# Kernel tuning notes

Hardware: AMD Instinct MI355X
Metric: run time of the kernel (lower is better)

The kernel has to match this reference:

```python
import jax, jax.numpy as jnp
import numpy as np

B, S, D = 2, 4096, 512
H, DQK, DV, W = 8, 64, 64, 32
ORDER = 6  # 2^(2*6)=4096 cells: 64x64 Hilbert grid covers max_seq_len=4096


def hilbert_d2xy(d, order):
    """Vectorized standard Hilbert curve d->(x,y) mapping on a 2^order grid."""
    x = jnp.zeros_like(d)
    y = jnp.zeros_like(d)
    t = d
    s = 1
    for _ in range(order):
        rx = (t // 2) & 1
        ry = (t ^ rx) & 1
        swap = ry == 0
        flip = swap & (rx == 1)
        xf = jnp.where(flip, s - 1 - x, x)
        yf = jnp.where(flip, s - 1 - y, y)
        x, y = jnp.where(swap, yf, xf), jnp.where(swap, xf, yf)
        x = x + s * rx
        y = y + s * ry
        t = t // 4
        s = s * 2
    return jnp.stack([x, y], axis=-1)


def neighbor_idx(seq_len, window):
    d = jnp.arange(seq_len, dtype=jnp.int32)
    coords = hilbert_d2xy(d, ORDER).astype(jnp.float32)  # (S, 2)
    diff = coords[:, None, :] - coords[None, :, :]
    dist = jnp.sqrt((diff ** 2).sum(-1))  # (S, S)
    _, idx = jax.lax.top_k(-dist, window)  # k smallest distances
    return idx.astype(jnp.int32)


def setup_inputs() -> dict:
    key = jax.random.key(0)
    k1, k2, k3, k4, k5 = jax.random.split(key, 5)
    sc = float(1.0 / np.sqrt(D))
    return {
        "x": jax.random.normal(k1, (B, S, D), jnp.float32),
        "W_q": jax.random.normal(k2, (H * DQK, D), jnp.float32) * sc,
        "W_k": jax.random.normal(k3, (H * DQK, D), jnp.float32) * sc,
        "W_v": jax.random.normal(k4, (H * DV, D), jnp.float32) * sc,
        "W_o": jax.random.normal(k5, (D, H * DV), jnp.float32) * sc,
        "neighbor_indices": neighbor_idx(S, W),
    }


def reference(x, W_q, W_k, W_v, W_o, neighbor_indices):
    b, s, _ = x.shape
    q = (x @ W_q.T).reshape(b, s, H, DQK).transpose(0, 2, 1, 3)  # (b,h,s,d)
    k = (x @ W_k.T).reshape(b, s, H, DQK).transpose(0, 2, 1, 3)
    v = (x @ W_v.T).reshape(b, s, H, DV).transpose(0, 2, 1, 3)
    kn = k[:, :, neighbor_indices, :]  # gather -> (b,h,s,w,d)
    vn = v[:, :, neighbor_indices, :]
    scale = float(1.0 / np.sqrt(DQK))
    scores = jnp.einsum('bhsd,bhswd->bhsw', q, kn) * scale
    attn = jax.nn.softmax(scores, axis=-1)
    out = jnp.einsum('bhsw,bhswd->bhsd', attn, vn)
    out = out.transpose(0, 2, 1, 3).reshape(b, s, H * DV)
    return out @ W_o.T
```

## Files before the change

kernel.cpp:

```cpp
#include <hip/hip_runtime.h>
#include <hip/hip_bf16.h>
#include <stdint.h>
#include <stddef.h>

constexpr int Bc = 2;
constexpr int Sc = 4096;
constexpr int Dc = 512;
constexpr int Hc = 8;
constexpr int Wc = 32;

using bf16_t = __bf16;
typedef __attribute__((ext_vector_type(8))) __bf16 bf16x8;
typedef __attribute__((ext_vector_type(4))) __bf16 bf16x4;
typedef __attribute__((ext_vector_type(2))) __bf16 bf16x2;
typedef __attribute__((ext_vector_type(4))) float f32x4;

__device__ __forceinline__ void async_copy16(const void* g, void* l) {
    __builtin_amdgcn_global_load_lds(
        (const __attribute__((address_space(1))) void*)g,
        (__attribute__((address_space(3))) void*)l,
        16, 0, 0);
}

__global__ void convert_all(const float* __restrict__ x,
                            const float* __restrict__ wq, const float* __restrict__ wk,
                            const float* __restrict__ wv, const float* __restrict__ wo,
                            bf16_t* __restrict__ xc, bf16_t* __restrict__ dq,
                            bf16_t* __restrict__ dk, bf16_t* __restrict__ dv,
                            bf16_t* __restrict__ dwo) {
    const int blk = blockIdx.x;
    const float* s; bf16_t* d; int base;
    if (blk < 4096) { s = x; d = xc; base = blk * 1024; }
    else {
        const int r = blk - 4096, which = r >> 8;
        s = (which == 0) ? wq : (which == 1) ? wk : (which == 2) ? wv : wo;
        d = (which == 0) ? dq : (which == 1) ? dk : (which == 2) ? dv : dwo;
        base = (r & 255) * 1024;
    }
    const int i = base + threadIdx.x * 4;
    const float4 v = *(const float4*)(s + i);
    bf16x4 o; o[0] = (bf16_t)v.x; o[1] = (bf16_t)v.y;
    o[2] = (bf16_t)v.z; o[3] = (bf16_t)v.w;
    *(bf16x4*)(d + i) = o;
}

template<int BM, int BN, int TM, int TN, bool F32OUT>
__global__ __launch_bounds__(256) void gemm_bt(
    const bf16_t* __restrict__ A, int lda,
    const bf16_t* __restrict__ B0, const bf16_t* __restrict__ B1,
    const bf16_t* __restrict__ B2, int ldb, int nPerB,
    void* __restrict__ C, int ldc, int K)
{
    constexpr int BK = 32;
    __shared__ __align__(1024) bf16_t Alds[BM * BK];
    __shared__ __align__(1024) bf16_t Blds[BN * BK];

    const int tid  = threadIdx.x;
    const int lane = tid & 63;
    const int wv   = tid >> 6;
    const int wm   = wv >> 1;
    const int wn   = wv & 1;
    const int r    = lane & 15;
    const int q4   = lane >> 4;

    const int blkM = blockIdx.x * BM;
    const int colC = blockIdx.y * BN;

    const bf16_t* Bp = B0;
    int nB = colC;
    if (nPerB > 0) {
        int wsel = colC / nPerB;
        nB = colC - wsel * nPerB;
        Bp = (wsel == 0) ? B0 : (wsel == 1) ? B1 : B2;
    }

    f32x4 acc[TM][TN];
    const f32x4 fzero = {0.f, 0.f, 0.f, 0.f};
    #pragma unroll
    for (int i = 0; i < TM; ++i)
        #pragma unroll
        for (int j = 0; j < TN; ++j) acc[i][j] = fzero;

    constexpr int A_LOADS = (BM * BK * 2) / (256 * 16);
    constexpr int B_LOADS = (BN * BK * 2) / (256 * 16);

    for (int kk = 0; kk < K; kk += BK) {
        __syncthreads();
        #pragma unroll
        for (int i = 0; i < A_LOADS; ++i) {
            int off  = i * 4096 + tid * 16;
            int row  = off >> 6;
            int colb = off & 63;
            const char* g = (const char*)A + ((size_t)(blkM + row) * lda + kk) * 2 + colb;
            async_copy16(g, (char*)Alds + off);
        }
        #pragma unroll
        for (int i = 0; i < B_LOADS; ++i) {
            int off  = i * 4096 + tid * 16;
            int row  = off >> 6;
            int colb = off & 63;
            const char* g = (const char*)Bp + ((size_t)(nB + row) * ldb + kk) * 2 + colb;
            async_copy16(g, (char*)Blds + off);
        }
        __syncthreads();

        bf16x8 af[TM], bfr[TN];
        #pragma unroll
        for (int mt = 0; mt < TM; ++mt)
            af[mt] = *(const bf16x8*)&Alds[(wm * TM * 16 + mt * 16 + r) * BK + q4 * 8];
        #pragma unroll
        for (int nt = 0; nt < TN; ++nt)
            bfr[nt] = *(const bf16x8*)&Blds[(wn * TN * 16 + nt * 16 + r) * BK + q4 * 8];

        #pragma unroll
        for (int mt = 0; mt < TM; ++mt)
            #pragma unroll
            for (int nt = 0; nt < TN; ++nt)
                acc[mt][nt] = __builtin_amdgcn_mfma_f32_16x16x32_bf16(
                    af[mt], bfr[nt], acc[mt][nt], 0, 0, 0);
    }

    #pragma unroll
    for (int mt = 0; mt < TM; ++mt) {
        #pragma unroll
        for (int nt = 0; nt < TN; ++nt) {
            int rr0 = blkM + wm * TM * 16 + mt * 16 + q4 * 4;
            int cc  = colC + wn * TN * 16 + nt * 16 + r;
            #pragma unroll
            for (int i = 0; i < 4; ++i) {
                size_t o = (size_t)(rr0 + i) * ldc + cc;
                if constexpr (F32OUT) ((float*)C)[o]  = acc[mt][nt][i];
                else                  ((bf16_t*)C)[o] = (bf16_t)acc[mt][nt][i];
            }
        }
    }
}

__global__ __launch_bounds__(256) void attn_fast(
    const bf16_t* __restrict__ QKV,
    const int*    __restrict__ nidx,
    bf16_t*       __restrict__ attn_out)
{
    __shared__ __align__(16) float wa_lds[4][64];
    const int lane = threadIdx.x & 63;
    const int wv   = threadIdx.x >> 6;

    const int bi  = blockIdx.x;
    const int blk = (bi & 7) * 2048 + (bi >> 3);
    const int wg  = blk * 4 + wv;
    const int s = wg & (Sc - 1);
    const int h = (wg >> 12) & (Hc - 1);
    const int b = wg >> 15;
    const size_t row = (size_t)b * Sc + s;

    const int w    = lane >> 1;
    const int half = lane & 1;
    const int t    = nidx[s * Wc + w];

    const char* qkvB = (const char*)QKV;
    const char* Qptr = qkvB + row * 3072 + h * 128 + half * 64;
    const char* Kptr = qkvB + ((size_t)b * Sc + t) * 3072 + 1024 + h * 128 + half * 64;

    bf16x8 q8[4], k8[4];
    #pragma unroll
    for (int i = 0; i < 4; ++i) {
        q8[i] = *(const bf16x8*)(Qptr + 16 * i);
        k8[i] = *(const bf16x8*)(Kptr + 16 * i);
    }
    float p = 0.f;
    #pragma unroll
    for (int i = 0; i < 4; ++i)
        #pragma unroll
        for (int j = 0; j < 8; ++j)
            p += (float)q8[i][j] * (float)k8[i][j];
    p += __shfl_xor(p, 1);
    p *= 0.125f;

    float mx = p;
    #pragma unroll
    for (int m = 2; m <= 32; m <<= 1) mx = fmaxf(mx, __shfl_xor(mx, m));
    const float e = __expf(p - mx);
    float sum = e;
    #pragma unroll
    for (int m = 2; m <= 32; m <<= 1) sum += __shfl_xor(sum, m);
    const float a = e / sum;

    if (half == 0) {
        wa_lds[wv][2 * w]     = __int_as_float(t * 3072);
        wa_lds[wv][2 * w + 1] = a;
    }
    __syncthreads();

    const int d2 = lane & 31;
    const int nh = lane >> 5;
    const float* chunkp = &wa_lds[wv][nh * 32];
    const char* Vb = qkvB + (size_t)b * Sc * 3072 + 2048 + h * 128;
    const int dk = d2 * 4;

    float acc0 = 0.f, acc1 = 0.f;
    #pragma unroll
    for (int j = 0; j < 8; ++j) {
        const float4 c = *(const float4*)(chunkp + 4 * j);
        {
            const unsigned v = *(const unsigned*)(Vb + __float_as_int(c.x) + dk);
            acc0 = fmaf(c.y, __uint_as_float(v << 16), acc0);
            acc1 = fmaf(c.y, __uint_as_float(v & 0xffff0000u), acc1);
        }
        {
            const unsigned v = *(const unsigned*)(Vb + __float_as_int(c.z) + dk);
            acc0 = fmaf(c.w, __uint_as_float(v << 16), acc0);
            acc1 = fmaf(c.w, __uint_as_float(v & 0xffff0000u), acc1);
        }
    }
    acc0 += __shfl_xor(acc0, 32);
    acc1 += __shfl_xor(acc1, 32);
    if (nh == 0) {
        bf16x2 pr; pr[0] = (bf16_t)acc0; pr[1] = (bf16_t)acc1;
        *(bf16x2*)((char*)attn_out + row * 1024 + h * 128 + dk) = pr;
    }
}

extern "C" void kernel_launch(void* const* d_in, const int* in_sizes, int n_in,
                              void* d_out, int out_size, void* d_ws, size_t ws_size,
                              hipStream_t stream) {
    (void)in_sizes; (void)n_in; (void)out_size; (void)ws_size;
    const int* nidx = (const int*)d_in[5];
    const int M = Bc * Sc;
    float* out = (float*)d_out;

    char* w = (char*)d_ws;
    bf16_t* xc   = (bf16_t*)(w + 256);
    bf16_t* Wqc  = xc  + 4194304;
    bf16_t* Wkc  = Wqc + 262144;
    bf16_t* Wvc  = Wkc + 262144;
    bf16_t* Woc  = Wvc + 262144;
    bf16_t* qkv  = Woc + 262144;
    bf16_t* attnS = xc;

    convert_all<<<5120, 256, 0, stream>>>(
        (const float*)d_in[0], (const float*)d_in[1], (const float*)d_in[2],
        (const float*)d_in[3], (const float*)d_in[4],
        xc, Wqc, Wkc, Wvc, Woc);

    gemm_bt<128, 128, 4, 4, false><<<dim3(M / 128, 1536 / 128), 256, 0, stream>>>(
        xc, Dc, Wqc, Wkc, Wvc, Dc, 512, qkv, 1536, Dc);

    attn_fast<<<(Bc * Hc * Sc) / 4, 256, 0, stream>>>(qkv, nidx, attnS);

    gemm_bt<128, 64, 4, 2, true><<<dim3(M / 128, 512 / 64), 256, 0, stream>>>(
        attnS, 512, Woc, Woc, Woc, 512, 0, out, Dc, Dc);
}
```

Baseline: 146.9 us.

## Restructure neighbor attention lane mapping, drop LDS and barrier, widen out-proj tile

The attention kernel now maps 8 lanes per neighbor over 16-byte dimension chunks, and each lane handles 4 neighbors. K and V are loaded as 16-byte vectors in the same pass. Softmax and the weighted V sum stay in registers using xor shuffles, so the LDS staging buffer and __syncthreads are removed. The output projection GEMM tile grows from 128x64 to 128x128, which halves its grid to 256 blocks and may reduce occupancy across CUs. The new path needs more shuffles to reduce the 8 accumulators.

```diff
diff --git a/kernel.cpp b/kernel.cpp
--- a/kernel.cpp
+++ b/kernel.cpp
@@ -141,7 +141,6 @@
     const int*    __restrict__ nidx,
     bf16_t*       __restrict__ attn_out)
 {
-    __shared__ __align__(16) float wa_lds[4][64];
     const int lane = threadIdx.x & 63;
     const int wv   = threadIdx.x >> 6;
 
@@ -153,70 +152,63 @@
     const int b = wg >> 15;
     const size_t row = (size_t)b * Sc + s;
 
-    const int w    = lane >> 1;
-    const int half = lane & 1;
-    const int t    = nidx[s * Wc + w];
-
-    const char* qkvB = (const char*)QKV;
-    const char* Qptr = qkvB + row * 3072 + h * 128 + half * 64;
-    const char* Kptr = qkvB + ((size_t)b * Sc + t) * 3072 + 1024 + h * 128 + half * 64;
-
-    bf16x8 q8[4], k8[4];
-    #pragma unroll
-    for (int i = 0; i < 4; ++i) {
-        q8[i] = *(const bf16x8*)(Qptr + 16 * i);
-        k8[i] = *(const bf16x8*)(Kptr + 16 * i);
-    }
-    float p = 0.f;
-    #pragma unroll
-    for (int i = 0; i < 4; ++i)
+    const int d8 = lane & 7;
+    const int wq = lane >> 3;
+
+    const char* qkvB  = (const char*)QKV;
+    const bf16x8 q8   = *(const bf16x8*)(qkvB + row * 3072 + h * 128 + d8 * 16);
+    const char* Kbase = qkvB + (size_t)b * Sc * 3072 + 1024 + h * 128 + d8 * 16;
+    const char* Vbase = qkvB + (size_t)b * Sc * 3072 + 2048 + h * 128 + d8 * 16;
+
+    float  p[4];
+    bf16x8 v8s[4];
+    #pragma unroll
+    for (int g = 0; g < 4; ++g) {
+        const int t = nidx[s * Wc + g * 8 + wq];
+        const size_t toff = (size_t)t * 3072;
+        const bf16x8 k8 = *(const bf16x8*)(Kbase + toff);
+        v8s[g] = *(const bf16x8*)(Vbase + toff);
+        float d = 0.f;
+        #pragma unroll
+        for (int j = 0; j < 8; ++j) d += (float)q8[j] * (float)k8[j];
+        d += __shfl_xor(d, 1);
+        d += __shfl_xor(d, 2);
+        d += __shfl_xor(d, 4);
+        p[g] = d * 0.125f;
+    }
+
+    float mx = fmaxf(fmaxf(p[0], p[1]), fmaxf(p[2], p[3]));
+    mx = fmaxf(mx, __shfl_xor(mx, 8));
+    mx = fmaxf(mx, __shfl_xor(mx, 16));
+    mx = fmaxf(mx, __shfl_xor(mx, 32));
+    float e[4];
+    float sum = 0.f;
+    #pragma unroll
+    for (int g = 0; g < 4; ++g) { e[g] = __expf(p[g] - mx); sum += e[g]; }
+    sum += __shfl_xor(sum, 8);
+    sum += __shfl_xor(sum, 16);
+    sum += __shfl_xor(sum, 32);
+    const float inv = 1.0f / sum;
+
+    float acc[8] = {0.f, 0.f, 0.f, 0.f, 0.f, 0.f, 0.f, 0.f};
+    #pragma unroll
+    for (int g = 0; g < 4; ++g) {
+        const float ag = e[g] * inv;
         #pragma unroll
         for (int j = 0; j < 8; ++j)
-            p += (float)q8[i][j] * (float)k8[i][j];
-    p += __shfl_xor(p, 1);
-    p *= 0.125f;
-
-    float mx = p;
-    #pragma unroll
-    for (int m = 2; m <= 32; m <<= 1) mx = fmaxf(mx, __shfl_xor(mx, m));
-    const float e = __expf(p - mx);
-    float sum = e;
-    #pragma unroll
-    for (int m = 2; m <= 32; m <<= 1) sum += __shfl_xor(sum, m);
-    const float a = e / sum;
-
-    if (half == 0) {
-        wa_lds[wv][2 * w]     = __int_as_float(t * 3072);
-        wa_lds[wv][2 * w + 1] = a;
-    }
-    __syncthreads();
-
-    const int d2 = lane & 31;
-    const int nh = lane >> 5;
-    const float* chunkp = &wa_lds[wv][nh * 32];
-    const char* Vb = qkvB + (size_t)b * Sc * 3072 + 2048 + h * 128;
-    const int dk = d2 * 4;
-
-    float acc0 = 0.f, acc1 = 0.f;
+            acc[j] = fmaf(ag, (float)v8s[g][j], acc[j]);
+    }
     #pragma unroll
     for (int j = 0; j < 8; ++j) {
-        const float4 c = *(const float4*)(chunkp + 4 * j);
-        {
-            const unsigned v = *(const unsigned*)(Vb + __float_as_int(c.x) + dk);
-            acc0 = fmaf(c.y, __uint_as_float(v << 16), acc0);
-            acc1 = fmaf(c.y, __uint_as_float(v & 0xffff0000u), acc1);
-        }
-        {
-            const unsigned v = *(const unsigned*)(Vb + __float_as_int(c.z) + dk);
-            acc0 = fmaf(c.w, __uint_as_float(v << 16), acc0);
-            acc1 = fmaf(c.w, __uint_as_float(v & 0xffff0000u), acc1);
-        }
-    }
-    acc0 += __shfl_xor(acc0, 32);
-    acc1 += __shfl_xor(acc1, 32);
-    if (nh == 0) {
-        bf16x2 pr; pr[0] = (bf16_t)acc0; pr[1] = (bf16_t)acc1;
-        *(bf16x2*)((char*)attn_out + row * 1024 + h * 128 + dk) = pr;
+        acc[j] += __shfl_xor(acc[j], 8);
+        acc[j] += __shfl_xor(acc[j], 16);
+        acc[j] += __shfl_xor(acc[j], 32);
+    }
+    if (wq == 0) {
+        bf16x8 o;
+        #pragma unroll
+        for (int j = 0; j < 8; ++j) o[j] = (bf16_t)acc[j];
+        *(bf16x8*)((char*)attn_out + row * 1024 + h * 128 + d8 * 16) = o;
     }
 }
 
@@ -247,6 +239,6 @@
 
     attn_fast<<<(Bc * Hc * Sc) / 4, 256, 0, stream>>>(qkv, nidx, attnS);
 
-    gemm_bt<128, 64, 4, 2, true><<<dim3(M / 128, 512 / 64), 256, 0, stream>>>(
+    gemm_bt<128, 128, 4, 4, true><<<dim3(M / 128, 512 / 128), 256, 0, stream>>>(
         attnS, 512, Woc, Woc, Woc, 512, 0, out, Dc, Dc);
 }
```

New measurement: 147.5 us. Within noise of the previous version (+0.4%).
